# Kernel optimization log

Measured on AMD Instinct MI355X. Metric: run time of the kernel, lower is better.

The kernel has to match this reference:

```python
import jax, jax.numpy as jnp
import numpy as np

B, L, D, H, FF, K = 2, 2048, 512, 16, 2048, 5
HD = D // H
EPS = 1e-5


def _ln(x, g, b):
    m = jnp.mean(x, axis=-1, keepdims=True)
    v = jnp.var(x, axis=-1, keepdims=True)
    return (x - m) / jnp.sqrt(v + EPS) * g + b


def _rope_table(seq_len, hd):
    pos = jnp.arange(seq_len, dtype=jnp.float32)
    inv = 1.0 / (10000.0 ** (jnp.arange(0, hd, 2, dtype=jnp.float32) / hd))
    ang = pos[:, None] * inv[None, :]            # [L, hd/2]
    return jnp.concatenate([jnp.cos(ang), jnp.sin(ang)], axis=-1)  # [L, hd]


def setup_inputs() -> dict:
    key = jax.random.key(0)
    ks = jax.random.split(key, 32)
    w = lambda k, shape: jax.random.normal(k, shape, jnp.float32) * 0.02
    z = lambda n: jnp.zeros((n,), jnp.float32)
    o = lambda n: jnp.ones((n,), jnp.float32)
    return {
        'src': jax.random.normal(ks[0], (B, L, D), jnp.float32),
        'Wq': w(ks[1], (D, D)), 'bq': z(D),
        'Wk': w(ks[2], (D, D)), 'bk': z(D),
        'Wv': w(ks[3], (D, D)), 'bv': z(D),
        'Wo': w(ks[4], (D, D)), 'bo': z(D),
        'ln_g': o(D), 'ln_b': z(D),
        'pw1_w': w(ks[5], (2 * D, D)), 'pw1_b': z(2 * D),
        'dw_w': w(ks[6], (D, 1, K)), 'dw_b': z(D),
        'bn_g': o(D), 'bn_b': z(D),
        'pw2_w': w(ks[7], (D, D)), 'pw2_b': z(D),
        'proj_w': w(ks[8], (L, L)), 'proj_b': z(L),
        'proj2_w': w(ks[9], (D, D)), 'proj2_b': z(D),
        'W1': w(ks[10], (FF, D)), 'b1': z(FF),
        'W2': w(ks[11], (D, FF)), 'b2': z(D),
        'n1_g': o(D), 'n1_b': z(D),
        'n2_g': o(D), 'n2_b': z(D),
    }


def reference(src, Wq, bq, Wk, bk, Wv, bv, Wo, bo, ln_g, ln_b,
              pw1_w, pw1_b, dw_w, dw_b, bn_g, bn_b, pw2_w, pw2_b,
              proj_w, proj_b, proj2_w, proj2_b, W1, b1, W2, b2,
              n1_g, n1_b, n2_g, n2_b):
    scale = HD ** -0.5
    pe = _rope_table(L, HD)
    c, s = pe[:, ::2], pe[:, 1::2]   # faithful to apply_RoPE's interleaved slicing of [cos|sin]

    def rope(x):  # x: [B,H,L,hd]
        xe, xo = x[..., ::2], x[..., 1::2]
        return jnp.concatenate([xe * c - xo * s, xe * s + xo * c], axis=-1)

    q = (src @ Wq.T + bq).reshape(B, L, H, HD).transpose(0, 2, 1, 3)
    k = (src @ Wk.T + bk).reshape(B, L, H, HD).transpose(0, 2, 1, 3)
    v = (src @ Wv.T + bv).reshape(B, L, H, HD).transpose(0, 2, 1, 3)
    q, k = rope(q), rope(k)

    slopes = jnp.asarray(2.0 ** (-(2.0 ** (-(np.log2(H) - 3.0))) * np.arange(H)), jnp.float32)
    idx = jnp.arange(L)
    dist = jnp.clip(idx[:, None] - idx[None, :], 0, None).astype(jnp.float32)
    alibi = slopes[:, None, None] * dist  # [H,L,L]

    scores = jnp.einsum('bhld,bhmd->bhlm', q, k) * scale + alibi[None]
    attn = jax.nn.softmax(scores, axis=-1)
    ctx = jnp.einsum('bhlm,bhmd->bhld', attn, v).transpose(0, 2, 1, 3).reshape(B, L, D)
    attn_out = ctx @ Wo.T + bo

    x0 = src + _ln(attn_out, n1_g, n1_b)

    # depthwise conformer conv block (stride=1, residual downsample = identity)
    x = _ln(x0, ln_g, ln_b)
    x = x @ pw1_w.T + pw1_b                      # [B,L,2D]
    a, g = x[..., :D], x[..., D:]
    x = a * jax.nn.sigmoid(g)                    # GLU
    x = x.transpose(0, 2, 1)                     # [B,D,L]
    x = jax.lax.conv_general_dilated(x, dw_w, (1,), [(K // 2, K // 2)],
                                     dimension_numbers=('NCH', 'OIH', 'NCH'),
                                     feature_group_count=D) + dw_b[None, :, None]
    x = x * (bn_g / jnp.sqrt(1.0 + EPS))[None, :, None] + bn_b[None, :, None]  # BN eval (mu=0, var=1)
    x = x * jnp.clip(x + 3.0, 0.0, 6.0) / 6.0    # hardswish
    conv = x.transpose(0, 2, 1) @ pw2_w.T + pw2_b + x0

    # seq-dim projection branch
    p = jnp.einsum('bld,ml->bmd', x0, proj_w) + proj_b[None, :, None]
    p = p @ proj2_w.T + proj2_b

    y = p + conv
    ff = jax.nn.gelu(y @ W1.T + b1, approximate=False) @ W2.T + b2
    return _ln(y + ff, n2_g, n2_b)
```

## Files before the change

### kernel.cpp

```cpp
#include <hip/hip_runtime.h>
#include <math.h>

#define B_ 2
#define L_ 2048
#define D_ 512
#define H_ 16
#define HD_ 32
#define FF_ 2048
#define BL_ 4096
#define EPS_ 1e-5f

typedef unsigned short ushort;
typedef unsigned int uint;
typedef __attribute__((ext_vector_type(8))) short bf16x8;
typedef __attribute__((ext_vector_type(4))) float f32x4;
typedef __attribute__((ext_vector_type(4))) uint u32x4;

__device__ __forceinline__ ushort bf16r(float f) {
  uint u = __float_as_uint(f);
  uint r = (u + 0x7FFFu + ((u >> 16) & 1u)) >> 16;
  return (ushort)r;
}
__device__ __forceinline__ float bf2f(uint u) { return __uint_as_float(u << 16); }

__device__ __forceinline__ float wsum(float v) {
#pragma unroll
  for (int o = 32; o; o >>= 1) v += __shfl_xor(v, o);
  return v;
}

__device__ __forceinline__ float gelu_fast(float x) {
  float t = x + 0.044715f * x * x * x;
  float e = exp2f(fminf(2.302118131f * t, 80.f));
  return x * e / (1.f + e);
}

__device__ __forceinline__ void gload16(const void* g, void* l) {
  __builtin_amdgcn_global_load_lds(
      (const __attribute__((address_space(1))) void*)g,
      (__attribute__((address_space(3))) void*)l, 16, 0, 0);
}

template <int TMv, int TNv, int EPI, int BROW, int GELU, int RES, int OUTF, int OUTB>
__global__ __launch_bounds__(256, 2) void gemm_bf_k(
    const ushort* __restrict__ A, const ushort* __restrict__ W,
    const float* __restrict__ bias, const float* __restrict__ res,
    float* __restrict__ Cf, ushort* __restrict__ Cb,
    const int M, const int N, const int Kd, const long sW, const long sC,
    const int ldC,
    const float* __restrict__ tab, ushort* __restrict__ Qb,
    ushort* __restrict__ Kb, ushort* __restrict__ Vb) {
  constexpr int MF = (TMv == 128) ? 4 : ((TNv == 128) ? 4 : 2);
  constexpr int NF = (TNv == 128) ? ((TMv == 128) ? 4 : 2) : 2;
  __shared__ __align__(16) ushort As[TMv * 64];
  __shared__ __align__(16) ushort Ws[TNv * 64];
  const int tid = threadIdx.x;
  const int wid = tid >> 6, lane = tid & 63;
  const int lane15 = lane & 15, lgrp = lane >> 4;
  const int rowoff = (TMv == 128) ? (wid >> 1) * 64
                                  : ((TNv == 64) ? (wid >> 1) * 32 : 0);
  const int wnoff = (TMv == 128) ? (wid & 1) * 64
                                 : ((TNv == 128) ? wid * 32 : (wid & 1) * 32);
  const int bm = blockIdx.y * TMv, bn = blockIdx.x * TNv;
  const int z = blockIdx.z;
  const ushort* Wz = W + (size_t)z * sW;

  f32x4 acc[MF][NF];
#pragma unroll
  for (int i = 0; i < MF; ++i)
#pragma unroll
    for (int j = 0; j < NF; ++j) acc[i][j] = (f32x4){0.f, 0.f, 0.f, 0.f};

  for (int k0 = 0; k0 < Kd; k0 += 64) {
    __syncthreads();
#pragma unroll
    for (int i = 0; i < TMv / 32; ++i) {
      const int cb = i * 256 + wid * 64;
      const int chunk = cb + lane;
      const int ml = chunk >> 3;
      const int c16 = (chunk & 7) ^ (ml & 7);
      gload16(A + (size_t)(bm + ml) * Kd + k0 + c16 * 8, &As[(size_t)cb * 8]);
    }
#pragma unroll
    for (int i = 0; i < TNv / 32; ++i) {
      const int cb = i * 256 + wid * 64;
      const int chunk = cb + lane;
      const int ml = chunk >> 3;
      const int c16 = (chunk & 7) ^ (ml & 7);
      gload16(Wz + (size_t)(bn + ml) * Kd + k0 + c16 * 8, &Ws[(size_t)cb * 8]);
    }
    __syncthreads();

    bf16x8 af[2][MF], wf[2][NF];
#pragma unroll
    for (int kk = 0; kk < 2; ++kk) {
#pragma unroll
      for (int f = 0; f < MF; ++f) {
        const int ma = rowoff + f * 16 + lane15;
        const int ca = (kk * 4 + lgrp) ^ (ma & 7);
        af[kk][f] = *(const bf16x8*)&As[ma * 64 + ca * 8];
      }
#pragma unroll
      for (int f = 0; f < NF; ++f) {
        const int nb = wnoff + f * 16 + lane15;
        const int cw = (kk * 4 + lgrp) ^ (nb & 7);
        wf[kk][f] = *(const bf16x8*)&Ws[nb * 64 + cw * 8];
      }
    }
#pragma unroll
    for (int kk = 0; kk < 2; ++kk)
#pragma unroll
      for (int fm = 0; fm < MF; ++fm)
#pragma unroll
        for (int fn = 0; fn < NF; ++fn)
          acc[fm][fn] = __builtin_amdgcn_mfma_f32_16x16x32_bf16(
              af[kk][fm], wf[kk][fn], acc[fm][fn], 0, 0, 0);
  }

#pragma unroll
  for (int fm = 0; fm < MF; ++fm) {
#pragma unroll
    for (int fn = 0; fn < NF; ++fn) {
      const int n = bn + wnoff + fn * 16 + lane15;
      float bcol = 0.f;
      if (EPI == 2) bcol = bias[(n >> 1) + (n & 1) * 512];
      else if (EPI == 1 || !BROW) bcol = bias[n];
#pragma unroll
      for (int r = 0; r < 4; ++r) {
        const int m = bm + rowoff + fm * 16 + lgrp * 4 + r;
        float val = acc[fm][fn][r];
        if (EPI == 1) {
          val += bcol;
          float p = __shfl_xor(val, 1);
          const int l = m & 2047, b = m >> 11;
          const int h = (n >> 5) & 15;
          if (n < 1024) {
            const int ch = n & 31, i2 = ch >> 1;
            const float cv = tab[l * 32 + i2], sv = tab[l * 32 + 16 + i2];
            const float o = (ch & 1) ? (p * sv + val * cv) : (val * cv - p * sv);
            const int dcol = (ch & 1) ? 16 + i2 : i2;
            if (n < 512)
              Qb[(((size_t)(b * 16 + h)) * 2048 + l) * 32 + dcol] =
                  bf16r(o * (0.1767766952966369f * 1.4426950408889634f));
            else
              Kb[(((size_t)(b * 16 + h)) * 2048 + l) * 32 + dcol] = bf16r(o);
          } else {
            Vb[(((size_t)(b * 16 + h)) * 2048 + l) * 32 + (n & 31)] = bf16r(val);
          }
        } else if (EPI == 2) {
          val += bcol;
          float p = __shfl_xor(val, 1);
          if (!(n & 1)) {
            float glu = val / (1.f + __expf(-p));
            Cb[(size_t)m * 512 + (n >> 1)] = bf16r(glu);
          }
        } else {
          val += BROW ? bias[m] : bcol;
          if (RES) val += res[(size_t)m * N + n];
          if (GELU) val = gelu_fast(val);
          const size_t o = (size_t)z * sC + (size_t)m * ldC + n;
          if (OUTF) Cf[o] = val;
          if (OUTB) Cb[o] = bf16r(val);
        }
      }
    }
  }
}

struct CvtArgs {
  const float* s[11];
  ushort* d[11];
  int n[11];
  int pm[11];
};
__global__ __launch_bounds__(256) void cvt_all_k(CvtArgs a) {
  const int seg = blockIdx.y;
  const int n = a.n[seg];
  const int i = (blockIdx.x * 256 + threadIdx.x) * 8;
  if (i >= n) return;
  const float* s = a.s[seg] + i;
  float4 x = *(const float4*)s, y = *(const float4*)(s + 4);
  bf16x8 o;
  o[0] = (short)bf16r(x.x); o[1] = (short)bf16r(x.y);
  o[2] = (short)bf16r(x.z); o[3] = (short)bf16r(x.w);
  o[4] = (short)bf16r(y.x); o[5] = (short)bf16r(y.y);
  o[6] = (short)bf16r(y.z); o[7] = (short)bf16r(y.w);
  ushort* d = a.d[seg] + i;
  const int pm = a.pm[seg];
  if (pm == 1) {
    int cc = i >> 3;
    int row = cc >> 6, off = cc & 63;
    int nrow = (row < 512) ? row * 2 : (row - 512) * 2 + 1;
    d = a.d[seg] + (((size_t)nrow << 6) + off) * 8;
  } else if (pm >= 2) {
    d = a.d[seg] + (size_t)(i >> 9) * 1024 + (i & 511) + ((pm == 3) ? 512 : 0);
  }
  *(bf16x8*)d = o;
}

__global__ void misc_k(float* __restrict__ tab, const float* __restrict__ bq,
                       const float* __restrict__ bk, const float* __restrict__ bv,
                       float* __restrict__ bqkv, const float* __restrict__ p2b,
                       const float* __restrict__ pw2b, float* __restrict__ bcat) {
  if (blockIdx.x < 128) {
    int t = blockIdx.x * 256 + threadIdx.x;
    int i = t & 15, l = t >> 4;
    float cv, sv;
    if (i < 8) {
      float inv0 = 1.0f / powf(10000.0f, (float)(2 * i) / 16.0f);
      float inv1 = 1.0f / powf(10000.0f, (float)(2 * i + 1) / 16.0f);
      cv = cosf((float)l * inv0);
      sv = cosf((float)l * inv1);
    } else {
      int ii = i - 8;
      float inv0 = 1.0f / powf(10000.0f, (float)(2 * ii) / 16.0f);
      float inv1 = 1.0f / powf(10000.0f, (float)(2 * ii + 1) / 16.0f);
      cv = sinf((float)l * inv0);
      sv = sinf((float)l * inv1);
    }
    tab[l * 32 + i] = cv;
    tab[l * 32 + 16 + i] = sv;
  } else {
    int i = threadIdx.x;
    bqkv[i] = bq[i];            bqkv[i + 256] = bq[i + 256];
    bqkv[512 + i] = bk[i];      bqkv[768 + i] = bk[i + 256];
    bqkv[1024 + i] = bv[i];     bqkv[1280 + i] = bv[i + 256];
    bcat[i] = p2b[i] + pw2b[i];
    bcat[i + 256] = p2b[i + 256] + pw2b[i + 256];
  }
}

__global__ __launch_bounds__(256) void transp_k(const float* __restrict__ x,
                                                ushort* __restrict__ xT) {
  __shared__ float t[32][33];
  const int b = blockIdx.z, l0 = blockIdx.x * 32, d0 = blockIdx.y * 32;
  const int tx = threadIdx.x & 31, ty = threadIdx.x >> 5;
#pragma unroll
  for (int i = 0; i < 4; ++i)
    t[ty + i * 8][tx] = x[((size_t)(b * L_ + l0 + ty + i * 8)) * D_ + d0 + tx];
  __syncthreads();
#pragma unroll
  for (int i = 0; i < 4; ++i)
    xT[((size_t)(b * D_ + d0 + ty + i * 8)) * L_ + l0 + tx] =
        bf16r(t[tx][ty + i * 8]);
}

__global__ __launch_bounds__(512, 4) void attn_mfma_k(const ushort* __restrict__ q,
                                                      const ushort* __restrict__ k,
                                                      const ushort* __restrict__ v,
                                                      ushort* __restrict__ ctx) {
  __shared__ __align__(16) ushort K_lds[4][130][8];
  __shared__ __align__(16) uint V_lds[32][68];
  const int tid = threadIdx.x;
  const int wid = tid >> 6, lane = tid & 63;
  const int s = lane >> 4, lr = lane & 15;
  const int bid = blockIdx.x;
  const int xcd = bid & 7, idx = bid >> 3;
  const int bh = xcd * 4 + (idx & 3);
  const int qt = idx >> 2;
  const int qb = qt * 128;
  const int h = bh & 15, bidx = bh >> 4;
  const float nslope = -exp2f(-0.5f * (float)h) * 1.4426950408889634f;
  const int qrow = qb + wid * 16 + lr;
  const float qgf = (float)qrow;
  const float cq = nslope * qgf;
  bf16x8 qa = *(const bf16x8*)&q[((size_t)bh * L_ + qrow) * HD_ + s * 8];

  bf16x8 vones;
#pragma unroll
  for (int i = 0; i < 8; ++i) vones[i] = (short)0x3F80;

  f32x4 acc0 = {0.f, 0.f, 0.f, 0.f}, acc1 = {0.f, 0.f, 0.f, 0.f};
  f32x4 accl = {0.f, 0.f, 0.f, 0.f};
  const ushort* kg = k + (size_t)bh * L_ * HD_;
  const ushort* vg = v + (size_t)bh * L_ * HD_;
  const int vslot = (lane & 48) + ((lane >> 1) & 3) * 4 + ((lane >> 3) & 1) * 2 + (lane & 1);
  const int kkey = tid >> 2, kslot = tid & 3;

  bf16x8 kreg;
  uint2 va, vb;
  {
    kreg = *(const bf16x8*)&kg[(size_t)kkey * HD_ + kslot * 8];
    const ushort* g0 = vg + (size_t)(2 * lane) * HD_ + wid * 4;
    va = *(const uint2*)g0;
    vb = *(const uint2*)(g0 + HD_);
  }

  for (int t0 = 0; t0 < L_; t0 += 128) {
    __syncthreads();
    *(bf16x8*)&K_lds[kslot][kkey][0] = kreg;
    V_lds[wid * 4 + 0][vslot] = __builtin_amdgcn_perm(vb.x, va.x, 0x05040100u);
    V_lds[wid * 4 + 1][vslot] = __builtin_amdgcn_perm(vb.x, va.x, 0x07060302u);
    V_lds[wid * 4 + 2][vslot] = __builtin_amdgcn_perm(vb.y, va.y, 0x05040100u);
    V_lds[wid * 4 + 3][vslot] = __builtin_amdgcn_perm(vb.y, va.y, 0x07060302u);
    if (t0 + 128 < L_) {
      kreg = *(const bf16x8*)&kg[(size_t)(t0 + 128 + kkey) * HD_ + kslot * 8];
      const ushort* g0 = vg + (size_t)(t0 + 128 + 2 * lane) * HD_ + wid * 4;
      va = *(const uint2*)g0;
      vb = *(const uint2*)(g0 + HD_);
    }
    asm volatile("s_waitcnt lgkmcnt(0)" ::: "memory");
    __builtin_amdgcn_s_barrier();
    __builtin_amdgcn_sched_barrier(0);

    f32x4 sc[8];
    __builtin_amdgcn_s_setprio(1);
#pragma unroll
    for (int c = 0; c < 8; ++c) {
      bf16x8 kf = *(const bf16x8*)&K_lds[s][c * 16 + lr][0];
      f32x4 zz = {0.f, 0.f, 0.f, 0.f};
      sc[c] = __builtin_amdgcn_mfma_f32_16x16x32_bf16(kf, qa, zz, 0, 0, 0);
    }
    __builtin_amdgcn_s_setprio(0);
    if (t0 < qb) {
      const float kb0 = (float)(t0 + s * 4);
#pragma unroll
      for (int c = 0; c < 8; ++c) {
        const float kc = kb0 + (float)(c * 16);
#pragma unroll
        for (int r = 0; r < 4; ++r)
          sc[c][r] = exp2f(fmaf(nslope, kc + (float)r, sc[c][r]));
      }
    } else if (t0 > qb) {
#pragma unroll
      for (int c = 0; c < 8; ++c)
#pragma unroll
        for (int r = 0; r < 4; ++r) sc[c][r] = exp2f(sc[c][r] + cq);
    } else {
      const float kb0 = (float)(t0 + s * 4);
#pragma unroll
      for (int c = 0; c < 8; ++c) {
        const float kc = kb0 + (float)(c * 16);
#pragma unroll
        for (int r = 0; r < 4; ++r) {
          float mn = fminf(kc + (float)r, qgf);
          sc[c][r] = exp2f(fmaf(nslope, mn, sc[c][r]));
        }
      }
    }
#pragma unroll
    for (int t = 0; t < 4; ++t) {
      uint w0 = __builtin_amdgcn_perm(__float_as_uint(sc[2 * t][1]),
                                      __float_as_uint(sc[2 * t][0]), 0x07060302u);
      uint w1 = __builtin_amdgcn_perm(__float_as_uint(sc[2 * t][3]),
                                      __float_as_uint(sc[2 * t][2]), 0x07060302u);
      uint w2 = __builtin_amdgcn_perm(__float_as_uint(sc[2 * t + 1][1]),
                                      __float_as_uint(sc[2 * t + 1][0]), 0x07060302u);
      uint w3 = __builtin_amdgcn_perm(__float_as_uint(sc[2 * t + 1][3]),
                                      __float_as_uint(sc[2 * t + 1][2]), 0x07060302u);
      u32x4 pw = {w0, w1, w2, w3};
      bf16x8 pf = __builtin_bit_cast(bf16x8, pw);
      bf16x8 v0 = *(const bf16x8*)&V_lds[lr][t * 16 + s * 4];
      bf16x8 v1 = *(const bf16x8*)&V_lds[16 + lr][t * 16 + s * 4];
      __builtin_amdgcn_s_setprio(1);
      acc0 = __builtin_amdgcn_mfma_f32_16x16x32_bf16(pf, v0, acc0, 0, 0, 0);
      acc1 = __builtin_amdgcn_mfma_f32_16x16x32_bf16(pf, v1, acc1, 0, 0, 0);
      accl = __builtin_amdgcn_mfma_f32_16x16x32_bf16(pf, vones, accl, 0, 0, 0);
      __builtin_amdgcn_s_setprio(0);
    }
  }
#pragma unroll
  for (int r = 0; r < 4; ++r) {
    float il = 1.f / accl[r];
    int qg2 = qb + wid * 16 + s * 4 + r;
    ushort* op = ctx + ((size_t)(bidx * L_ + qg2)) * D_ + h * HD_;
    op[lr] = bf16r(acc0[r] * il);
    op[16 + lr] = bf16r(acc1[r] * il);
  }
}

__global__ __launch_bounds__(64) void ln_res_ln_k(
    const float* __restrict__ x, const float* __restrict__ res,
    const float* __restrict__ g1, const float* __restrict__ b1,
    const float* __restrict__ g2, const float* __restrict__ b2,
    float* __restrict__ x0, ushort* __restrict__ xln) {
  int row = blockIdx.x, lane = threadIdx.x;
  const float* xr = x + (size_t)row * D_;
  float v[8];
  float s = 0.f, ss = 0.f;
#pragma unroll
  for (int i = 0; i < 8; ++i) {
    float t = xr[i * 64 + lane];
    v[i] = t; s += t; ss += t * t;
  }
  s = wsum(s); ss = wsum(ss);
  float mean = s * (1.f / 512.f);
  float rstd = rsqrtf(ss * (1.f / 512.f) - mean * mean + EPS_);
  float w[8];
  float s2 = 0.f, ss2 = 0.f;
#pragma unroll
  for (int i = 0; i < 8; ++i) {
    int idx = i * 64 + lane;
    float t = res[(size_t)row * D_ + idx] + (v[i] - mean) * rstd * g1[idx] + b1[idx];
    w[i] = t; s2 += t; ss2 += t * t;
  }
  s2 = wsum(s2); ss2 = wsum(ss2);
  float mean2 = s2 * (1.f / 512.f);
  float rstd2 = rsqrtf(ss2 * (1.f / 512.f) - mean2 * mean2 + EPS_);
#pragma unroll
  for (int i = 0; i < 8; ++i) {
    int idx = i * 64 + lane;
    x0[(size_t)row * D_ + idx] = w[i];
    xln[(size_t)row * D_ + idx] = bf16r((w[i] - mean2) * rstd2 * g2[idx] + b2[idx]);
  }
}

__global__ __launch_bounds__(64) void ln_k(const float* __restrict__ x,
                                           const float* __restrict__ g,
                                           const float* __restrict__ bb,
                                           float* __restrict__ out) {
  int row = blockIdx.x, lane = threadIdx.x;
  const float* xr = x + (size_t)row * D_;
  float v[8];
  float s = 0.f, ss = 0.f;
#pragma unroll
  for (int i = 0; i < 8; ++i) {
    float t = xr[i * 64 + lane];
    v[i] = t; s += t; ss += t * t;
  }
  s = wsum(s); ss = wsum(ss);
  float mean = s * (1.f / 512.f);
  float rstd = rsqrtf(ss * (1.f / 512.f) - mean * mean + EPS_);
#pragma unroll
  for (int i = 0; i < 8; ++i) {
    int idx = i * 64 + lane;
    out[(size_t)row * D_ + idx] = (v[i] - mean) * rstd * g[idx] + bb[idx];
  }
}

__global__ __launch_bounds__(256) void convbn_k(
    const ushort* __restrict__ x, const float* __restrict__ w,
    const float* __restrict__ wb, const float* __restrict__ bng,
    const float* __restrict__ bnb, ushort* __restrict__ out) {
  int t = blockIdx.x * 256 + threadIdx.x;
  int c4 = t & 127;
  int l = (t >> 7) & 2047;
  int b = t >> 18;
  int d0 = c4 * 4;
  float accv[4] = {0.f, 0.f, 0.f, 0.f};
#pragma unroll
  for (int kt = 0; kt < 5; ++kt) {
    int ls = l + kt - 2;
    if (ls >= 0 && ls < L_) {
      uint2 xv = *(const uint2*)&x[((size_t)(b * L_ + ls)) * D_ + d0];
      float pv[4] = {bf2f(xv.x & 0xffffu), bf2f(xv.x >> 16),
                     bf2f(xv.y & 0xffffu), bf2f(xv.y >> 16)};
#pragma unroll
      for (int j = 0; j < 4; ++j) accv[j] += pv[j] * w[(d0 + j) * 5 + kt];
    }
  }
  const float bscale = rsqrtf(1.0f + EPS_);
  float po[4];
#pragma unroll
  for (int j = 0; j < 4; ++j) {
    int d = d0 + j;
    float vv = accv[j] + wb[d];
    vv = vv * (bng[d] * bscale) + bnb[d];
    float hs = fminf(fmaxf(vv + 3.f, 0.f), 6.f);
    po[j] = vv * hs * (1.f / 6.f);
  }
  uint lo = (uint)bf16r(po[0]) | ((uint)bf16r(po[1]) << 16);
  uint hi = (uint)bf16r(po[2]) | ((uint)bf16r(po[3]) << 16);
  uint2 o2 = {lo, hi};
  *(uint2*)&out[((size_t)(b * L_ + l)) * 1024 + d0] = o2;
}

extern "C" void kernel_launch(void* const* d_in, const int* in_sizes, int n_in,
                              void* d_out, int out_size, void* d_ws, size_t ws_size,
                              hipStream_t stream) {
  const float* src    = (const float*)d_in[0];
  const float* Wq     = (const float*)d_in[1];
  const float* bq     = (const float*)d_in[2];
  const float* Wk     = (const float*)d_in[3];
  const float* bk     = (const float*)d_in[4];
  const float* Wv     = (const float*)d_in[5];
  const float* bv     = (const float*)d_in[6];
  const float* Wo     = (const float*)d_in[7];
  const float* bo     = (const float*)d_in[8];
  const float* ln_g   = (const float*)d_in[9];
  const float* ln_b   = (const float*)d_in[10];
  const float* pw1_w  = (const float*)d_in[11];
  const float* pw1_b  = (const float*)d_in[12];
  const float* dw_w   = (const float*)d_in[13];
  const float* dw_b   = (const float*)d_in[14];
  const float* bn_g   = (const float*)d_in[15];
  const float* bn_b   = (const float*)d_in[16];
  const float* pw2_w  = (const float*)d_in[17];
  const float* pw2_b  = (const float*)d_in[18];
  const float* proj_w = (const float*)d_in[19];
  const float* proj_b = (const float*)d_in[20];
  const float* proj2_w= (const float*)d_in[21];
  const float* proj2_b= (const float*)d_in[22];
  const float* W1     = (const float*)d_in[23];
  const float* b1     = (const float*)d_in[24];
  const float* W2     = (const float*)d_in[25];
  const float* b2     = (const float*)d_in[26];
  const float* n1_g   = (const float*)d_in[27];
  const float* n1_b   = (const float*)d_in[28];
  const float* n2_g   = (const float*)d_in[29];
  const float* n2_b   = (const float*)d_in[30];
  float* out = (float*)d_out;

  char* wsb = (char*)d_ws;
  const size_t MB1 = 1 << 20;
  ushort* wqkv = (ushort*)(wsb);
  ushort* wo_w = (ushort*)(wsb + 1536 * 1024);
  ushort* pw1w = (ushort*)(wsb + 2 * MB1);
  ushort* wcat = (ushort*)(wsb + 3 * MB1);
  ushort* pjww = (ushort*)(wsb + 4 * MB1);
  ushort* w1w  = (ushort*)(wsb + 12 * MB1);
  ushort* w2w  = (ushort*)(wsb + 14 * MB1);
  float*  bqkv = (float*)(wsb + 16 * MB1);
  float*  bcat = (float*)(wsb + 16 * MB1 + 6144);
  float*  tab  = (float*)(wsb + 16 * MB1 + 8192);
  char* A0 = wsb + 17 * MB1;
  ushort* src_bf = (ushort*)A0;
  ushort* ff_bf  = (ushort*)A0;
  float*  x0     = (float*)(A0 + 8 * MB1);
  char* B0 = A0 + 16 * MB1;
  ushort* Qb = (ushort*)B0;
  ushort* Kb = (ushort*)(B0 + 4 * MB1);
  ushort* Vb = (ushort*)(B0 + 8 * MB1);
  ushort* glu_bf = (ushort*)B0;
  ushort* xln_bf = (ushort*)(B0 + 8 * MB1);
  ushort* cat_bf = (ushort*)(B0 + 4 * MB1);
  float*  zbuf   = (float*)B0;
  char* C0 = B0 + 12 * MB1;
  ushort* ctx_bf = (ushort*)C0;
  ushort* x0T    = (ushort*)C0;
  ushort* y_bf   = (ushort*)C0;
  char* D0 = C0 + 4 * MB1;
  float* attnout = (float*)D0;
  float* y       = (float*)D0;

  dim3 blk(256);

  CvtArgs ca;
  for (int i = 0; i < 11; ++i) ca.pm[i] = 0;
  ca.s[0] = Wq;     ca.d[0] = wqkv;              ca.n[0] = 512 * 512;
  ca.s[1] = Wk;     ca.d[1] = wqkv + 512 * 512;  ca.n[1] = 512 * 512;
  ca.s[2] = Wv;     ca.d[2] = wqkv + 1024 * 512; ca.n[2] = 512 * 512;
  ca.s[3] = Wo;     ca.d[3] = wo_w;              ca.n[3] = 512 * 512;
  ca.s[4] = pw1_w;  ca.d[4] = pw1w;              ca.n[4] = 1024 * 512; ca.pm[4] = 1;
  ca.s[5] = pw2_w;  ca.d[5] = wcat;              ca.n[5] = 512 * 512;  ca.pm[5] = 3;
  ca.s[6] = proj_w; ca.d[6] = pjww;              ca.n[6] = 2048 * 2048;
  ca.s[7] = proj2_w;ca.d[7] = wcat;              ca.n[7] = 512 * 512;  ca.pm[7] = 2;
  ca.s[8] = W1;     ca.d[8] = w1w;               ca.n[8] = 2048 * 512;
  ca.s[9] = W2;     ca.d[9] = w2w;               ca.n[9] = 512 * 2048;
  ca.s[10]= src;    ca.d[10]= src_bf;            ca.n[10]= BL_ * D_;
  cvt_all_k<<<dim3(2048, 11), blk, 0, stream>>>(ca);
  misc_k<<<dim3(129), blk, 0, stream>>>(tab, bq, bk, bv, bqkv, proj2_b, pw2_b, bcat);

  gemm_bf_k<64,128,1,0,0,0,0,0><<<dim3(12, 64), blk, 0, stream>>>(
      src_bf, wqkv, bqkv, nullptr, nullptr, nullptr,
      BL_, 1536, 512, 0, 0, 1536, tab, Qb, Kb, Vb);

  attn_mfma_k<<<dim3(512), dim3(512), 0, stream>>>(Qb, Kb, Vb, ctx_bf);

  gemm_bf_k<64,64,0,0,0,0,1,0><<<dim3(8, 64), blk, 0, stream>>>(
      ctx_bf, wo_w, bo, nullptr, attnout, nullptr,
      BL_, 512, 512, 0, 0, 512, nullptr, nullptr, nullptr, nullptr);

  ln_res_ln_k<<<BL_, 64, 0, stream>>>(attnout, src, n1_g, n1_b, ln_g, ln_b,
                                      x0, xln_bf);

  transp_k<<<dim3(64, 16, 2), blk, 0, stream>>>(x0, x0T);

  gemm_bf_k<64,128,2,0,0,0,0,1><<<dim3(8, 64), blk, 0, stream>>>(
      xln_bf, pw1w, pw1_b, nullptr, nullptr, glu_bf,
      BL_, 1024, 512, 0, 0, 512, nullptr, nullptr, nullptr, nullptr);

  convbn_k<<<(B_ * L_ * (D_ / 4)) / 256, blk, 0, stream>>>(
      glu_bf, dw_w, dw_b, bn_g, bn_b, cat_bf + 512);

  gemm_bf_k<64,64,0,1,0,0,0,1><<<dim3(8, 32, 2), blk, 0, stream>>>(
      pjww, x0T, proj_b, nullptr, nullptr, cat_bf,
      2048, 512, 2048, (long)512 * 2048, (long)2048 * 1024, 1024,
      nullptr, nullptr, nullptr, nullptr);

  gemm_bf_k<64,64,0,0,0,1,1,1><<<dim3(8, 64), blk, 0, stream>>>(
      cat_bf, wcat, bcat, x0, y, y_bf,
      BL_, 512, 1024, 0, 0, 512, nullptr, nullptr, nullptr, nullptr);

  gemm_bf_k<64,128,0,0,1,0,0,1><<<dim3(16, 64), blk, 0, stream>>>(
      y_bf, w1w, b1, nullptr, nullptr, ff_bf,
      BL_, 2048, 512, 0, 0, 2048, nullptr, nullptr, nullptr, nullptr);

  gemm_bf_k<64,64,0,0,0,1,1,0><<<dim3(8, 64), blk, 0, stream>>>(
      ff_bf, w2w, b2, y, zbuf, nullptr,
      BL_, 512, 2048, 0, 0, 512, nullptr, nullptr, nullptr, nullptr);

  ln_k<<<BL_, 64, 0, stream>>>(zbuf, n2_g, n2_b, out);
}
```

Measured before the change: 221.0 us.

## Split-K the seq projection and FFN down GEMMs, reduce partials in follow-up kernels

Adds a split-K mode to the bf16 GEMM template, splitting the K dimension in two halves across grid z. It is applied to the sequence-projection GEMM (K=2048) and the FFN second GEMM (K=2048). Each GEMM writes partial sums that a new small kernel combines: one adds the proj partials plus row bias into the concat buffer, and the final LayerNorm now sums the two FFN partials with bias and residual. The aim is to double the block count for these long-K GEMMs to improve CU occupancy, at the cost of an extra launch, extra partial-buffer traffic, and bf16 rounding of the proj partials.

```diff
diff --git a/kernel.cpp b/kernel.cpp
--- a/kernel.cpp
+++ b/kernel.cpp
@@ -41,7 +41,7 @@
       (__attribute__((address_space(3))) void*)l, 16, 0, 0);
 }
 
-template <int TMv, int TNv, int EPI, int BROW, int GELU, int RES, int OUTF, int OUTB>
+template <int TMv, int TNv, int EPI, int BROW, int GELU, int RES, int OUTF, int OUTB, int SPK>
 __global__ __launch_bounds__(256, 2) void gemm_bf_k(
     const ushort* __restrict__ A, const ushort* __restrict__ W,
     const float* __restrict__ bias, const float* __restrict__ res,
@@ -63,7 +63,11 @@
                                  : ((TNv == 128) ? wid * 32 : (wid & 1) * 32);
   const int bm = blockIdx.y * TMv, bn = blockIdx.x * TNv;
   const int z = blockIdx.z;
-  const ushort* Wz = W + (size_t)z * sW;
+  const int lda = SPK ? (Kd << 1) : Kd;
+  const int kh = SPK ? (z & 1) : 0;
+  const int zb = SPK ? (z >> 1) : z;
+  const ushort* Az = A + (size_t)kh * Kd;
+  const ushort* Wz = W + (size_t)zb * sW + (size_t)kh * Kd;
 
   f32x4 acc[MF][NF];
 #pragma unroll
@@ -79,7 +83,7 @@
       const int chunk = cb + lane;
       const int ml = chunk >> 3;
       const int c16 = (chunk & 7) ^ (ml & 7);
-      gload16(A + (size_t)(bm + ml) * Kd + k0 + c16 * 8, &As[(size_t)cb * 8]);
+      gload16(Az + (size_t)(bm + ml) * lda + k0 + c16 * 8, &As[(size_t)cb * 8]);
     }
 #pragma unroll
     for (int i = 0; i < TNv / 32; ++i) {
@@ -87,7 +91,7 @@
       const int chunk = cb + lane;
       const int ml = chunk >> 3;
       const int c16 = (chunk & 7) ^ (ml & 7);
-      gload16(Wz + (size_t)(bn + ml) * Kd + k0 + c16 * 8, &Ws[(size_t)cb * 8]);
+      gload16(Wz + (size_t)(bn + ml) * lda + k0 + c16 * 8, &Ws[(size_t)cb * 8]);
     }
     __syncthreads();
 
@@ -124,7 +128,7 @@
       const int n = bn + wnoff + fn * 16 + lane15;
       float bcol = 0.f;
       if (EPI == 2) bcol = bias[(n >> 1) + (n & 1) * 512];
-      else if (EPI == 1 || !BROW) bcol = bias[n];
+      else if ((EPI == 1 || !BROW) && bias) bcol = bias[n];
 #pragma unroll
       for (int r = 0; r < 4; ++r) {
         const int m = bm + rowoff + fm * 16 + lgrp * 4 + r;
@@ -155,7 +159,7 @@
             Cb[(size_t)m * 512 + (n >> 1)] = bf16r(glu);
           }
         } else {
-          val += BROW ? bias[m] : bcol;
+          val += BROW ? (bias ? bias[m] : 0.f) : bcol;
           if (RES) val += res[(size_t)m * N + n];
           if (GELU) val = gelu_fast(val);
           const size_t o = (size_t)z * sC + (size_t)m * ldC + n;
@@ -245,6 +249,27 @@
         bf16r(t[tx][ty + i * 8]);
 }
 
+__global__ __launch_bounds__(256) void cmb_proj_k(const ushort* __restrict__ p,
+                                                  const float* __restrict__ biasRow,
+                                                  ushort* __restrict__ cat) {
+  int t = blockIdx.x * 256 + threadIdx.x;
+  int n4 = t & 127;
+  int m = (t >> 7) & 2047;
+  int zb = t >> 18;
+  size_t i0 = ((size_t)(zb * 2) * 2048 + m) * 512 + n4 * 4;
+  uint2 a = *(const uint2*)&p[i0];
+  uint2 b = *(const uint2*)&p[i0 + (size_t)2048 * 512];
+  float bm = biasRow[m];
+  float o0 = bf2f(a.x & 0xffffu) + bf2f(b.x & 0xffffu) + bm;
+  float o1 = bf2f(a.x >> 16) + bf2f(b.x >> 16) + bm;
+  float o2 = bf2f(a.y & 0xffffu) + bf2f(b.y & 0xffffu) + bm;
+  float o3 = bf2f(a.y >> 16) + bf2f(b.y >> 16) + bm;
+  uint lo = (uint)bf16r(o0) | ((uint)bf16r(o1) << 16);
+  uint hi = (uint)bf16r(o2) | ((uint)bf16r(o3) << 16);
+  uint2 ov = {lo, hi};
+  *(uint2*)&cat[((size_t)(zb * 2048 + m)) * 1024 + n4 * 4] = ov;
+}
+
 __global__ __launch_bounds__(512, 4) void attn_mfma_k(const ushort* __restrict__ q,
                                                       const ushort* __restrict__ k,
                                                       const ushort* __restrict__ v,
@@ -405,17 +430,21 @@
   }
 }
 
-__global__ __launch_bounds__(64) void ln_k(const float* __restrict__ x,
-                                           const float* __restrict__ g,
-                                           const float* __restrict__ bb,
-                                           float* __restrict__ out) {
+__global__ __launch_bounds__(64) void ln2_k(const float* __restrict__ zA,
+                                            const float* __restrict__ zB,
+                                            const float* __restrict__ yres,
+                                            const float* __restrict__ b2,
+                                            const float* __restrict__ g,
+                                            const float* __restrict__ bb,
+                                            float* __restrict__ out) {
   int row = blockIdx.x, lane = threadIdx.x;
-  const float* xr = x + (size_t)row * D_;
+  const size_t base = (size_t)row * D_;
   float v[8];
   float s = 0.f, ss = 0.f;
 #pragma unroll
   for (int i = 0; i < 8; ++i) {
-    float t = xr[i * 64 + lane];
+    int idx = i * 64 + lane;
+    float t = zA[base + idx] + zB[base + idx] + b2[idx] + yres[base + idx];
     v[i] = t; s += t; ss += t * t;
   }
   s = wsum(s); ss = wsum(ss);
@@ -424,7 +453,7 @@
 #pragma unroll
   for (int i = 0; i < 8; ++i) {
     int idx = i * 64 + lane;
-    out[(size_t)row * D_ + idx] = (v[i] - mean) * rstd * g[idx] + bb[idx];
+    out[base + idx] = (v[i] - mean) * rstd * g[idx] + bb[idx];
   }
 }
 
@@ -515,6 +544,7 @@
   float*  tab  = (float*)(wsb + 16 * MB1 + 8192);
   char* A0 = wsb + 17 * MB1;
   ushort* src_bf = (ushort*)A0;
+  ushort* pprt   = (ushort*)A0;
   ushort* ff_bf  = (ushort*)A0;
   float*  x0     = (float*)(A0 + 8 * MB1);
   char* B0 = A0 + 16 * MB1;
@@ -524,7 +554,7 @@
   ushort* glu_bf = (ushort*)B0;
   ushort* xln_bf = (ushort*)(B0 + 8 * MB1);
   ushort* cat_bf = (ushort*)(B0 + 4 * MB1);
-  float*  zbuf   = (float*)B0;
+  float*  zprt   = (float*)B0;
   char* C0 = B0 + 12 * MB1;
   ushort* ctx_bf = (ushort*)C0;
   ushort* x0T    = (ushort*)C0;
@@ -551,13 +581,13 @@
   cvt_all_k<<<dim3(2048, 11), blk, 0, stream>>>(ca);
   misc_k<<<dim3(129), blk, 0, stream>>>(tab, bq, bk, bv, bqkv, proj2_b, pw2_b, bcat);
 
-  gemm_bf_k<64,128,1,0,0,0,0,0><<<dim3(12, 64), blk, 0, stream>>>(
+  gemm_bf_k<64,128,1,0,0,0,0,0,0><<<dim3(12, 64), blk, 0, stream>>>(
       src_bf, wqkv, bqkv, nullptr, nullptr, nullptr,
       BL_, 1536, 512, 0, 0, 1536, tab, Qb, Kb, Vb);
 
   attn_mfma_k<<<dim3(512), dim3(512), 0, stream>>>(Qb, Kb, Vb, ctx_bf);
 
-  gemm_bf_k<64,64,0,0,0,0,1,0><<<dim3(8, 64), blk, 0, stream>>>(
+  gemm_bf_k<64,64,0,0,0,0,1,0,0><<<dim3(8, 64), blk, 0, stream>>>(
       ctx_bf, wo_w, bo, nullptr, attnout, nullptr,
       BL_, 512, 512, 0, 0, 512, nullptr, nullptr, nullptr, nullptr);
 
@@ -566,29 +596,32 @@
 
   transp_k<<<dim3(64, 16, 2), blk, 0, stream>>>(x0, x0T);
 
-  gemm_bf_k<64,128,2,0,0,0,0,1><<<dim3(8, 64), blk, 0, stream>>>(
+  gemm_bf_k<64,128,2,0,0,0,0,1,0><<<dim3(8, 64), blk, 0, stream>>>(
       xln_bf, pw1w, pw1_b, nullptr, nullptr, glu_bf,
       BL_, 1024, 512, 0, 0, 512, nullptr, nullptr, nullptr, nullptr);
 
   convbn_k<<<(B_ * L_ * (D_ / 4)) / 256, blk, 0, stream>>>(
       glu_bf, dw_w, dw_b, bn_g, bn_b, cat_bf + 512);
 
-  gemm_bf_k<64,64,0,1,0,0,0,1><<<dim3(8, 32, 2), blk, 0, stream>>>(
-      pjww, x0T, proj_b, nullptr, nullptr, cat_bf,
-      2048, 512, 2048, (long)512 * 2048, (long)2048 * 1024, 1024,
+  gemm_bf_k<64,64,0,0,0,0,0,1,1><<<dim3(8, 32, 4), blk, 0, stream>>>(
+      pjww, x0T, nullptr, nullptr, nullptr, pprt,
+      2048, 512, 1024, (long)512 * 2048, (long)2048 * 512, 512,
       nullptr, nullptr, nullptr, nullptr);
-
-  gemm_bf_k<64,64,0,0,0,1,1,1><<<dim3(8, 64), blk, 0, stream>>>(
+  cmb_proj_k<<<dim3(2048), blk, 0, stream>>>(pprt, proj_b, cat_bf);
+
+  gemm_bf_k<64,64,0,0,0,1,1,1,0><<<dim3(8, 64), blk, 0, stream>>>(
       cat_bf, wcat, bcat, x0, y, y_bf,
       BL_, 512, 1024, 0, 0, 512, nullptr, nullptr, nullptr, nullptr);
 
-  gemm_bf_k<64,128,0,0,1,0,0,1><<<dim3(16, 64), blk, 0, stream>>>(
+  gemm_bf_k<64,128,0,0,1,0,0,1,0><<<dim3(16, 64), blk, 0, stream>>>(
       y_bf, w1w, b1, nullptr, nullptr, ff_bf,
       BL_, 2048, 512, 0, 0, 2048, nullptr, nullptr, nullptr, nullptr);
 
-  gemm_bf_k<64,64,0,0,0,1,1,0><<<dim3(8, 64), blk, 0, stream>>>(
-      ff_bf, w2w, b2, y, zbuf, nullptr,
-      BL_, 512, 2048, 0, 0, 512, nullptr, nullptr, nullptr, nullptr);
-
-  ln_k<<<BL_, 64, 0, stream>>>(zbuf, n2_g, n2_b, out);
-}
+  gemm_bf_k<64,64,0,0,0,0,1,0,1><<<dim3(8, 64, 2), blk, 0, stream>>>(
+      ff_bf, w2w, nullptr, nullptr, zprt, nullptr,
+      BL_, 512, 1024, 0, (long)BL_ * 512, 512,
+      nullptr, nullptr, nullptr, nullptr);
+
+  ln2_k<<<BL_, 64, 0, stream>>>(zprt, zprt + (size_t)BL_ * 512, y, b2,
+                                n2_g, n2_b, out);
+}
```

Result: no change. 220.2 us (-0.3%).
